# Performance work log

Measured on AMD Instinct MI355X. Metric: run time of the kernel, lower is better.

Reference implementation:

```python
import jax, jax.numpy as jnp
from jax import lax
import numpy as np

NUM_TAGS = 17
B, S = 2048, 512


def setup_inputs() -> dict:
    key = jax.random.key(0)
    k1, k2, k3, k4, k5 = jax.random.split(key, 5)
    inputs = jax.random.normal(k1, (B, S, NUM_TAGS), dtype=jnp.float32)
    tags = jax.random.randint(k2, (B, S), 0, NUM_TAGS, dtype=jnp.int64)
    mask = jnp.ones((B, S), dtype=jnp.int32)
    # learned CRF parameters (xavier-ish / normal init like the torch module)
    transitions = jax.random.normal(k3, (NUM_TAGS, NUM_TAGS), dtype=jnp.float32) * (2.0 / NUM_TAGS) ** 0.5
    start_transitions = jax.random.normal(k4, (NUM_TAGS,), dtype=jnp.float32)
    end_transitions = jax.random.normal(k5, (NUM_TAGS,), dtype=jnp.float32)
    return {"inputs": inputs, "tags": tags, "mask": mask,
            "transitions": transitions,
            "start_transitions": start_transitions,
            "end_transitions": end_transitions}


def _crf_loss(inputs, tags, mask, transitions, start_transitions, end_transitions):
    b, s, t = inputs.shape
    maskf = mask.astype(inputs.dtype)  # (B,S)

    # ---- log partition (denominator): sequential forward recurrence ----
    alpha0 = inputs[:, 0] + start_transitions[None, :]  # (B,T)

    def step(alpha, xm):
        logit_t, m_t = xm  # (B,T), (B,)
        # inner[b,i,j] = alpha[b,i] + emit[b,j] + trans[i,j]
        inner = alpha[:, :, None] + logit_t[:, None, :] + transitions[None, :, :]
        new_alpha = jax.nn.logsumexp(inner, axis=1)  # (B,T)
        alpha = new_alpha * m_t[:, None] + alpha * (1.0 - m_t)[:, None]
        return alpha, None

    xs = (jnp.swapaxes(inputs, 0, 1)[1:], jnp.swapaxes(maskf, 0, 1)[1:])  # (S-1,B,T),(S-1,B)
    alpha, _ = lax.scan(step, alpha0, xs)
    log_denominator = jax.nn.logsumexp(alpha + end_transitions[None, :], axis=-1)  # (B,)

    # ---- gold path score (numerator), fully vectorized over time ----
    score = start_transitions[tags[:, 0]]  # (B,)
    trans_sc = transitions[tags[:, :-1], tags[:, 1:]]  # (B,S-1)
    emit_sc = jnp.take_along_axis(inputs[:, :-1], tags[:, :-1, None], axis=2)[..., 0]  # (B,S-1)
    score = score + jnp.sum(trans_sc * maskf[:, 1:] + emit_sc * maskf[:, :-1], axis=1)
    last_idx = jnp.sum(mask, axis=1).astype(jnp.int32) - 1  # (B,)
    last_tags = jnp.take_along_axis(tags, last_idx[:, None].astype(tags.dtype), axis=1)[:, 0]
    last_input = jnp.take_along_axis(inputs[:, -1], last_tags[:, None], axis=1)[:, 0]
    score = score + end_transitions[last_tags] + last_input * maskf[:, -1]

    return jnp.sum(score - log_denominator)


def reference(inputs, tags, mask, transitions, start_transitions, end_transitions):
    return _crf_loss(inputs, tags, mask, transitions, start_transitions, end_transitions)
```

## Files before the change

### kernel.cpp

```cpp
#include <hip/hip_runtime.h>

#define B_ 2048
#define S_ 512
#define T_ 17
#define REC 40
#define FWDB 64
#define MAINB 128

typedef float v16f __attribute__((ext_vector_type(16)));
typedef short v8s  __attribute__((ext_vector_type(8)));
typedef float f4u  __attribute__((ext_vector_type(4), aligned(4)));

union frag_u { unsigned u[4]; v8s v; };

static __device__ inline unsigned pkbf(float lo, float hi) {
    unsigned r;
    asm volatile("v_cvt_pk_bf16_f32 %0, %1, %2" : "=v"(r) : "v"(lo), "v"(hi));
    return r;
}

#define LOADK(Q0, Q1, SS, MM, T0_) do {                                      \
    const float* bp_ = ip + (size_t)(T0_) * T_;                              \
    _Pragma("unroll") for (int u_ = 0; u_ < 4; ++u_) {                       \
        Q0[u_] = *(const f4u*)(bp_ + u_ * T_ + 4 * h);                       \
        Q1[u_] = *(const f4u*)(bp_ + u_ * T_ + 8 + 4 * h);                   \
        SS[u_] = bp_[u_ * T_ + 16];                                          \
    }                                                                        \
    MM = *(const int4*)(mp + (T0_));                                         \
} while (0)

#define PACKB(S0,S1,S2,S3,S4,S5,S6,S7, BOUT) do {                            \
    unsigned P0_ = pkbf(S0, S1), P1_ = pkbf(S2, S3);                         \
    unsigned R0_ = pkbf(S4, S5), R1_ = pkbf(S6, S7);                         \
    auto s0_ = __builtin_amdgcn_permlane32_swap(P0_, R0_, false, false);     \
    auto s1_ = __builtin_amdgcn_permlane32_swap(P1_, R1_, false, false);     \
    BOUT.u[0] = s0_[0]; BOUT.u[1] = s1_[0];                                  \
    BOUT.u[2] = s0_[1]; BOUT.u[3] = s1_[1];                                  \
} while (0)

#define W16SWAP() do {                                                       \
    auto rw_ = __builtin_amdgcn_permlane32_swap(__float_as_uint(W8),         \
                                                __float_as_uint(W8),         \
                                                false, false);               \
    w16 = __uint_as_float(rw_[0]);                                           \
} while (0)

#define FSTEP(Q0u, Q1u, Su, Mu) do {                                         \
    frag_u Bf_;                                                              \
    PACKB(W0,W1,W2,W3,W4,W5,W6,W7, Bf_);                                     \
    v16f acc_ = __builtin_amdgcn_mfma_f32_32x32x16_bf16(A1.v, Bf_.v, zacc,0,0,0); \
    float d0_=__expf((Q0u).x), d1_=__expf((Q0u).y);                          \
    float d2_=__expf((Q0u).z), d3_=__expf((Q0u).w);                          \
    float d4_=__expf((Q1u).x), d5_=__expf((Q1u).y);                          \
    float d6_=__expf((Q1u).z), d7_=__expf((Q1u).w);                          \
    float d8_=__expf(Su);                                                    \
    bool bm_ = (Mu) != 0;                                                    \
    float n0_ = fmaf(E16[0], w16, acc_[0]) * d0_;                            \
    float n1_ = fmaf(E16[1], w16, acc_[1]) * d1_;                            \
    float n2_ = fmaf(E16[2], w16, acc_[2]) * d2_;                            \
    float n3_ = fmaf(E16[3], w16, acc_[3]) * d3_;                            \
    float n4_ = fmaf(E16[4], w16, acc_[4]) * d4_;                            \
    float n5_ = fmaf(E16[5], w16, acc_[5]) * d5_;                            \
    float n6_ = fmaf(E16[6], w16, acc_[6]) * d6_;                            \
    float n7_ = fmaf(E16[7], w16, acc_[7]) * d7_;                            \
    float n8_ = fmaf(E16[8], w16, acc_[8]) * d8_;                            \
    W0=bm_?n0_:W0; W1=bm_?n1_:W1; W2=bm_?n2_:W2; W3=bm_?n3_:W3;              \
    W4=bm_?n4_:W4; W5=bm_?n5_:W5; W6=bm_?n6_:W6; W7=bm_?n7_:W7;              \
    W8=bm_?n8_:W8;                                                           \
    W16SWAP();                                                               \
} while (0)

#define BSTEP(Q0u, Q1u, Su, Mu) do {                                         \
    float d0_=__expf((Q0u).x), d1_=__expf((Q0u).y);                          \
    float d2_=__expf((Q0u).z), d3_=__expf((Q0u).w);                          \
    float d4_=__expf((Q1u).x), d5_=__expf((Q1u).y);                          \
    float d6_=__expf((Q1u).z), d7_=__expf((Q1u).w);                          \
    float d8_=__expf(Su);                                                    \
    float U16_ = w16 * d8_;                                                  \
    frag_u Bf_;                                                              \
    PACKB(W0*d0_, W1*d1_, W2*d2_, W3*d3_,                                    \
          W4*d4_, W5*d5_, W6*d6_, W7*d7_, Bf_);                              \
    v16f acc_ = __builtin_amdgcn_mfma_f32_32x32x16_bf16(A1.v, Bf_.v, zacc,0,0,0); \
    bool bm_ = (Mu) != 0;                                                    \
    float n0_ = fmaf(E16[0], U16_, acc_[0]);                                 \
    float n1_ = fmaf(E16[1], U16_, acc_[1]);                                 \
    float n2_ = fmaf(E16[2], U16_, acc_[2]);                                 \
    float n3_ = fmaf(E16[3], U16_, acc_[3]);                                 \
    float n4_ = fmaf(E16[4], U16_, acc_[4]);                                 \
    float n5_ = fmaf(E16[5], U16_, acc_[5]);                                 \
    float n6_ = fmaf(E16[6], U16_, acc_[6]);                                 \
    float n7_ = fmaf(E16[7], U16_, acc_[7]);                                 \
    float n8_ = fmaf(E16[8], U16_, acc_[8]);                                 \
    W0=bm_?n0_:W0; W1=bm_?n1_:W1; W2=bm_?n2_:W2; W3=bm_?n3_:W3;              \
    W4=bm_?n4_:W4; W5=bm_?n5_:W5; W6=bm_?n6_:W6; W7=bm_?n7_:W7;              \
    W8=bm_?n8_:W8;                                                           \
    W16SWAP();                                                               \
} while (0)

#define RENORM() do {                                                        \
    float M_ = fmaxf(fmaxf(fmaxf(W0,W1),fmaxf(W2,W3)),                       \
                     fmaxf(fmaxf(W4,W5),fmaxf(fmaxf(W6,W7),W8)));            \
    auto rm_ = __builtin_amdgcn_permlane32_swap(__float_as_uint(M_),         \
                                                __float_as_uint(M_),         \
                                                false, false);               \
    M_ = fmaxf(__uint_as_float(rm_[0]), __uint_as_float(rm_[1]));            \
    float r_ = 1.0f / M_;                                                    \
    Z += __logf(M_);                                                         \
    W0*=r_; W1*=r_; W2*=r_; W3*=r_; W4*=r_;                                  \
    W5*=r_; W6*=r_; W7*=r_; W8*=r_; w16*=r_;                                 \
} while (0)

#define FCHUNK(Q0a, Q1a, Sa, Ma) do {                                        \
    FSTEP(Q0a[0], Q1a[0], Sa[0], (Ma).x);                                    \
    FSTEP(Q0a[1], Q1a[1], Sa[1], (Ma).y);                                    \
    FSTEP(Q0a[2], Q1a[2], Sa[2], (Ma).z);                                    \
    FSTEP(Q0a[3], Q1a[3], Sa[3], (Ma).w);                                    \
    RENORM();                                                                \
} while (0)

#define BCHUNK(Q0a, Q1a, Sa, Ma) do {                                        \
    BSTEP(Q0a[3], Q1a[3], Sa[3], (Ma).w);                                    \
    BSTEP(Q0a[2], Q1a[2], Sa[2], (Ma).z);                                    \
    BSTEP(Q0a[1], Q1a[1], Sa[1], (Ma).y);                                    \
    BSTEP(Q0a[0], Q1a[0], Sa[0], (Ma).x);                                    \
    RENORM();                                                                \
} while (0)

__global__ __launch_bounds__(64) void crf_fused(
    const float* __restrict__ inputs,
    const int*   __restrict__ tags,
    const int*   __restrict__ mask,
    const float* __restrict__ trans,
    const float* __restrict__ startt,
    const float* __restrict__ endt,
    float* __restrict__ ws)
{
    __shared__ float tl[T_ * T_];
    const int lane = (int)threadIdx.x;
    const int bid = (int)blockIdx.x;
    for (int k = lane; k < T_ * T_; k += 64) tl[k] = trans[k];
    __syncthreads();

    if (bid < MAINB) {
        const bool isF = (bid < FWDB);
        const int h = lane >> 5;
        const int col = lane & 31;
        const int seq = (isF ? bid : bid - FWDB) * 32 + col;

        frag_u A1;
#pragma unroll
        for (int wd = 0; wd < 4; ++wd) {
            const int k0 = 8 * h + 2 * wd, k1 = k0 + 1;
            float e0 = 0.0f, e1 = 0.0f;
            if (col < 17) {
                e0 = isF ? __expf(tl[k0 * T_ + col]) : __expf(tl[col * T_ + k0]);
                e1 = isF ? __expf(tl[k1 * T_ + col]) : __expf(tl[col * T_ + k1]);
            }
            A1.u[wd] = pkbf(e0, e1);
        }
        float E16[9];
#pragma unroll
        for (int k = 0; k < 4; ++k) {
            const int r0 = 4 * h + k, r1 = 8 + 4 * h + k;
            E16[k]     = __expf(isF ? tl[16 * T_ + r0] : tl[r0 * T_ + 16]);
            E16[4 + k] = __expf(isF ? tl[16 * T_ + r1] : tl[r1 * T_ + 16]);
        }
        E16[8] = (h == 0) ? __expf(tl[16 * T_ + 16]) : 0.0f;

        v16f zacc;
#pragma unroll
        for (int r = 0; r < 16; ++r) zacc[r] = 0.0f;

        const float* ip = inputs + (size_t)seq * (S_ * T_);
        const int*   mp = mask + (size_t)seq * S_;

        float W0, W1, W2, W3, W4, W5, W6, W7, W8, w16, Z = 0.0f;

        f4u X0[4], X1[4]; float XS[4]; int4 XM;
        f4u Y0[4], Y1[4]; float YS[4]; int4 YM;

        if (isF) {
            LOADK(X0, X1, XS, XM, 0);
            LOADK(Y0, Y1, YS, YM, 4);
            {
                f4u s0 = *(const f4u*)(startt + 4 * h);
                f4u s1 = *(const f4u*)(startt + 8 + 4 * h);
                W0 = __expf(X0[0].x + s0.x); W1 = __expf(X0[0].y + s0.y);
                W2 = __expf(X0[0].z + s0.z); W3 = __expf(X0[0].w + s0.w);
                W4 = __expf(X1[0].x + s1.x); W5 = __expf(X1[0].y + s1.y);
                W6 = __expf(X1[0].z + s1.z); W7 = __expf(X1[0].w + s1.w);
                W8 = h ? 0.0f : __expf(XS[0] + startt[16]);
                W16SWAP();
            }
            FSTEP(X0[1], X1[1], XS[1], XM.y);
            FSTEP(X0[2], X1[2], XS[2], XM.z);
            FSTEP(X0[3], X1[3], XS[3], XM.w);
            RENORM();
            LOADK(X0, X1, XS, XM, 8);
            FCHUNK(Y0, Y1, YS, YM);
            for (int cp = 1; cp < 31; ++cp) {
                LOADK(Y0, Y1, YS, YM, 8 * cp + 4);
                FCHUNK(X0, X1, XS, XM);
                LOADK(X0, X1, XS, XM, 8 * cp + 8);
                FCHUNK(Y0, Y1, YS, YM);
            }
            LOADK(Y0, Y1, YS, YM, 252);
            FCHUNK(X0, X1, XS, XM);
            FCHUNK(Y0, Y1, YS, YM);
            float* rec = ws + (size_t)seq * REC;
            rec[4*h+0] = W0; rec[4*h+1] = W1; rec[4*h+2] = W2; rec[4*h+3] = W3;
            rec[8+4*h+0] = W4; rec[8+4*h+1] = W5; rec[8+4*h+2] = W6; rec[8+4*h+3] = W7;
            if (h == 0) { rec[16] = W8; rec[17] = Z; }
        } else {
            LOADK(X0, X1, XS, XM, 508);
            LOADK(Y0, Y1, YS, YM, 504);
            {
                f4u e0 = *(const f4u*)(endt + 4 * h);
                f4u e1 = *(const f4u*)(endt + 8 + 4 * h);
                W0 = __expf(e0.x); W1 = __expf(e0.y);
                W2 = __expf(e0.z); W3 = __expf(e0.w);
                W4 = __expf(e1.x); W5 = __expf(e1.y);
                W6 = __expf(e1.z); W7 = __expf(e1.w);
                W8 = h ? 0.0f : __expf(endt[16]);
                W16SWAP();
            }
            BCHUNK(X0, X1, XS, XM);
            LOADK(X0, X1, XS, XM, 500);
            BCHUNK(Y0, Y1, YS, YM);
            for (int cp = 1; cp < 31; ++cp) {
                LOADK(Y0, Y1, YS, YM, 508 - 8 * cp - 4);
                BCHUNK(X0, X1, XS, XM);
                LOADK(X0, X1, XS, XM, 508 - 8 * cp - 8);
                BCHUNK(Y0, Y1, YS, YM);
            }
            LOADK(Y0, Y1, YS, YM, 256);
            BCHUNK(X0, X1, XS, XM);
            BCHUNK(Y0, Y1, YS, YM);
            float* rec = ws + (size_t)seq * REC;
            rec[18+4*h+0] = W0; rec[18+4*h+1] = W1;
            rec[18+4*h+2] = W2; rec[18+4*h+3] = W3;
            rec[18+8+4*h+0] = W4; rec[18+8+4*h+1] = W5;
            rec[18+8+4*h+2] = W6; rec[18+8+4*h+3] = W7;
            if (h == 0) { rec[34] = W8; rec[35] = Z; }
        }
    } else {
        const int s = bid - MAINB;
        const int* tp = tags + (size_t)s * S_;
        const int* mp = mask + (size_t)s * S_;
        const float* ib = inputs + (size_t)s * (S_ * T_);
        const int4* tp4 = (const int4*)tp;
        const int4* mp4 = (const int4*)mp;

        int4 t0 = tp4[2 * lane], t1 = tp4[2 * lane + 1];
        int4 m0 = mp4[2 * lane], m1 = mp4[2 * lane + 1];
        int tg[8] = {t0.x, t0.y, t0.z, t0.w, t1.x, t1.y, t1.z, t1.w};
        int mi[8] = {m0.x, m0.y, m0.z, m0.w, m1.x, m1.y, m1.z, m1.w};
        int tprev = (lane > 0) ? tp[8 * lane - 1] : 0;

        float e = 0.0f, tr = 0.0f;
        int ms = 0;
#pragma unroll
        for (int u = 0; u < 8; ++u) {
            int t = 8 * lane + u;
            float mf = (float)mi[u];
            float gate = (t <= S_ - 2) ? mf : 0.0f;
            e = fmaf(gate, ib[(size_t)t * T_ + tg[u]], e);
            int pt = (u == 0) ? tprev : tg[u - 1];
            float tv = tl[pt * T_ + tg[u]];
            tr = fmaf((t >= 1) ? mf : 0.0f, tv, tr);
            ms += mi[u];
        }
        for (int d = 1; d < 64; d <<= 1) {
            e  += __shfl_xor(e, d);
            tr += __shfl_xor(tr, d);
            ms += __shfl_xor(ms, d);
        }
        if (lane == 0) {
            int li = ms - 1; if (li < 0) li = 0;
            int lt = tp[li];
            float ml = (float)mp[S_ - 1];
            float lin = ib[(size_t)(S_ - 1) * T_ + lt];
            float sc = startt[tp[0]] + tr + e + endt[lt] + lin * ml;
            ws[(size_t)s * REC + 36] = sc;
        }
    }
}

__global__ __launch_bounds__(256) void crf_final(const float* __restrict__ ws,
                                                 float* __restrict__ out)
{
    __shared__ float sm[256];
    const int tid = (int)threadIdx.x;
    float a = 0.0f;
    for (int s = tid; s < B_; s += 256) {
        const float* r = ws + (size_t)s * REC;
        float dot = 0.0f;
#pragma unroll
        for (int i = 0; i < T_; ++i) dot = fmaf(r[i], r[18 + i], dot);
        a += r[36] - (r[17] + r[35] + __logf(dot));
    }
    sm[tid] = a;
    __syncthreads();
    for (int k = 128; k >= 1; k >>= 1) {
        if (tid < k) sm[tid] += sm[tid + k];
        __syncthreads();
    }
    if (tid == 0) out[0] = sm[0];
}

extern "C" void kernel_launch(void* const* d_in, const int* in_sizes, int n_in,
                              void* d_out, int out_size, void* d_ws, size_t ws_size,
                              hipStream_t stream)
{
    const float* inputs = (const float*)d_in[0];
    const int*   tags   = (const int*)d_in[1];
    const int*   mask   = (const int*)d_in[2];
    const float* trans  = (const float*)d_in[3];
    const float* startt = (const float*)d_in[4];
    const float* endt   = (const float*)d_in[5];
    float* out = (float*)d_out;
    float* ws  = (float*)d_ws;

    crf_fused<<<MAINB + B_, 64, 0, stream>>>(inputs, tags, mask, trans,
                                             startt, endt, ws);
    crf_final<<<1, 256, 0, stream>>>(ws, out);
}
```

Measured before the change: 67.93 us.

## Interleave forward and backward CRF recurrences in one wavefront

Instead of separate blocks running the forward half and the backward half of each sequence, each wave now runs both chains and alternates their steps. The two independent dependency chains (MFMA, exp, permlane) can then hide each other's latency, and the recurrence needs half as many blocks. The asm volatile qualifier is dropped from the bf16 pack so the compiler can schedule it. The cost is roughly doubled register pressure per wave and fewer waves in flight on the GPU.

```diff
diff --git a/kernel.cpp b/kernel.cpp
--- a/kernel.cpp
+++ b/kernel.cpp
@@ -4,8 +4,7 @@
 #define S_ 512
 #define T_ 17
 #define REC 40
-#define FWDB 64
-#define MAINB 128
+#define MAINB 64
 
 typedef float v16f __attribute__((ext_vector_type(16)));
 typedef short v8s  __attribute__((ext_vector_type(8)));
@@ -15,11 +14,76 @@
 
 static __device__ inline unsigned pkbf(float lo, float hi) {
     unsigned r;
-    asm volatile("v_cvt_pk_bf16_f32 %0, %1, %2" : "=v"(r) : "v"(lo), "v"(hi));
+    asm("v_cvt_pk_bf16_f32 %0, %1, %2" : "=v"(r) : "v"(lo), "v"(hi));
     return r;
 }
 
-#define LOADK(Q0, Q1, SS, MM, T0_) do {                                      \
+#define PACKB(S0,S1,S2,S3,S4,S5,S6,S7, BOUT) do {                            \
+    unsigned P0_ = pkbf(S0, S1), P1_ = pkbf(S2, S3);                         \
+    unsigned R0_ = pkbf(S4, S5), R1_ = pkbf(S6, S7);                         \
+    auto s0_ = __builtin_amdgcn_permlane32_swap(P0_, R0_, false, false);     \
+    auto s1_ = __builtin_amdgcn_permlane32_swap(P1_, R1_, false, false);     \
+    BOUT.u[0] = s0_[0]; BOUT.u[1] = s1_[0];                                  \
+    BOUT.u[2] = s0_[1]; BOUT.u[3] = s1_[1];                                  \
+} while (0)
+
+#define W16SWAPA(W, w16) do {                                                \
+    auto rw_ = __builtin_amdgcn_permlane32_swap(__float_as_uint(W[8]),       \
+                                                __float_as_uint(W[8]),       \
+                                                false, false);               \
+    w16 = __uint_as_float(rw_[0]);                                           \
+} while (0)
+
+#define EXP9(dd_, Q0u, Q1u, Su) do {                                         \
+    dd_[0]=__expf((Q0u).x); dd_[1]=__expf((Q0u).y);                          \
+    dd_[2]=__expf((Q0u).z); dd_[3]=__expf((Q0u).w);                          \
+    dd_[4]=__expf((Q1u).x); dd_[5]=__expf((Q1u).y);                          \
+    dd_[6]=__expf((Q1u).z); dd_[7]=__expf((Q1u).w);                          \
+    dd_[8]=__expf(Su);                                                       \
+} while (0)
+
+#define FSTEPA(W, w16, Z, A1, E16, Q0u, Q1u, Su, Mu) do {                    \
+    frag_u Bf_;                                                              \
+    PACKB(W[0],W[1],W[2],W[3],W[4],W[5],W[6],W[7], Bf_);                     \
+    v16f acc_ = __builtin_amdgcn_mfma_f32_32x32x16_bf16(A1.v, Bf_.v, zacc,0,0,0); \
+    float dd_[9]; EXP9(dd_, Q0u, Q1u, Su);                                   \
+    bool bm_ = (Mu) != 0;                                                    \
+    _Pragma("unroll") for (int k_ = 0; k_ < 9; ++k_) {                       \
+        float n_ = fmaf(E16[k_], w16, acc_[k_]) * dd_[k_];                   \
+        W[k_] = bm_ ? n_ : W[k_];                                            \
+    }                                                                        \
+    W16SWAPA(W, w16);                                                        \
+} while (0)
+
+#define BSTEPA(W, w16, Z, A1, E16, Q0u, Q1u, Su, Mu) do {                    \
+    float dd_[9]; EXP9(dd_, Q0u, Q1u, Su);                                   \
+    float U16_ = w16 * dd_[8];                                               \
+    frag_u Bf_;                                                              \
+    PACKB(W[0]*dd_[0], W[1]*dd_[1], W[2]*dd_[2], W[3]*dd_[3],                \
+          W[4]*dd_[4], W[5]*dd_[5], W[6]*dd_[6], W[7]*dd_[7], Bf_);          \
+    v16f acc_ = __builtin_amdgcn_mfma_f32_32x32x16_bf16(A1.v, Bf_.v, zacc,0,0,0); \
+    bool bm_ = (Mu) != 0;                                                    \
+    _Pragma("unroll") for (int k_ = 0; k_ < 9; ++k_) {                       \
+        float n_ = fmaf(E16[k_], U16_, acc_[k_]);                            \
+        W[k_] = bm_ ? n_ : W[k_];                                            \
+    }                                                                        \
+    W16SWAPA(W, w16);                                                        \
+} while (0)
+
+#define RENORMA(W, w16, Z) do {                                              \
+    float M_ = fmaxf(fmaxf(fmaxf(W[0],W[1]),fmaxf(W[2],W[3])),               \
+                     fmaxf(fmaxf(W[4],W[5]),fmaxf(fmaxf(W[6],W[7]),W[8])));  \
+    auto rm_ = __builtin_amdgcn_permlane32_swap(__float_as_uint(M_),         \
+                                                __float_as_uint(M_),         \
+                                                false, false);               \
+    M_ = fmaxf(__uint_as_float(rm_[0]), __uint_as_float(rm_[1]));            \
+    float r_ = 1.0f / M_;                                                    \
+    Z += __logf(M_);                                                         \
+    _Pragma("unroll") for (int k_ = 0; k_ < 9; ++k_) W[k_] *= r_;            \
+    w16 *= r_;                                                               \
+} while (0)
+
+#define LOADC(Q0, Q1, SS, MM, T0_) do {                                      \
     const float* bp_ = ip + (size_t)(T0_) * T_;                              \
     _Pragma("unroll") for (int u_ = 0; u_ < 4; ++u_) {                       \
         Q0[u_] = *(const f4u*)(bp_ + u_ * T_ + 4 * h);                       \
@@ -29,104 +93,28 @@
     MM = *(const int4*)(mp + (T0_));                                         \
 } while (0)
 
-#define PACKB(S0,S1,S2,S3,S4,S5,S6,S7, BOUT) do {                            \
-    unsigned P0_ = pkbf(S0, S1), P1_ = pkbf(S2, S3);                         \
-    unsigned R0_ = pkbf(S4, S5), R1_ = pkbf(S6, S7);                         \
-    auto s0_ = __builtin_amdgcn_permlane32_swap(P0_, R0_, false, false);     \
-    auto s1_ = __builtin_amdgcn_permlane32_swap(P1_, R1_, false, false);     \
-    BOUT.u[0] = s0_[0]; BOUT.u[1] = s1_[0];                                  \
-    BOUT.u[2] = s0_[1]; BOUT.u[3] = s1_[1];                                  \
-} while (0)
-
-#define W16SWAP() do {                                                       \
-    auto rw_ = __builtin_amdgcn_permlane32_swap(__float_as_uint(W8),         \
-                                                __float_as_uint(W8),         \
-                                                false, false);               \
-    w16 = __uint_as_float(rw_[0]);                                           \
-} while (0)
-
-#define FSTEP(Q0u, Q1u, Su, Mu) do {                                         \
-    frag_u Bf_;                                                              \
-    PACKB(W0,W1,W2,W3,W4,W5,W6,W7, Bf_);                                     \
-    v16f acc_ = __builtin_amdgcn_mfma_f32_32x32x16_bf16(A1.v, Bf_.v, zacc,0,0,0); \
-    float d0_=__expf((Q0u).x), d1_=__expf((Q0u).y);                          \
-    float d2_=__expf((Q0u).z), d3_=__expf((Q0u).w);                          \
-    float d4_=__expf((Q1u).x), d5_=__expf((Q1u).y);                          \
-    float d6_=__expf((Q1u).z), d7_=__expf((Q1u).w);                          \
-    float d8_=__expf(Su);                                                    \
-    bool bm_ = (Mu) != 0;                                                    \
-    float n0_ = fmaf(E16[0], w16, acc_[0]) * d0_;                            \
-    float n1_ = fmaf(E16[1], w16, acc_[1]) * d1_;                            \
-    float n2_ = fmaf(E16[2], w16, acc_[2]) * d2_;                            \
-    float n3_ = fmaf(E16[3], w16, acc_[3]) * d3_;                            \
-    float n4_ = fmaf(E16[4], w16, acc_[4]) * d4_;                            \
-    float n5_ = fmaf(E16[5], w16, acc_[5]) * d5_;                            \
-    float n6_ = fmaf(E16[6], w16, acc_[6]) * d6_;                            \
-    float n7_ = fmaf(E16[7], w16, acc_[7]) * d7_;                            \
-    float n8_ = fmaf(E16[8], w16, acc_[8]) * d8_;                            \
-    W0=bm_?n0_:W0; W1=bm_?n1_:W1; W2=bm_?n2_:W2; W3=bm_?n3_:W3;              \
-    W4=bm_?n4_:W4; W5=bm_?n5_:W5; W6=bm_?n6_:W6; W7=bm_?n7_:W7;              \
-    W8=bm_?n8_:W8;                                                           \
-    W16SWAP();                                                               \
-} while (0)
-
-#define BSTEP(Q0u, Q1u, Su, Mu) do {                                         \
-    float d0_=__expf((Q0u).x), d1_=__expf((Q0u).y);                          \
-    float d2_=__expf((Q0u).z), d3_=__expf((Q0u).w);                          \
-    float d4_=__expf((Q1u).x), d5_=__expf((Q1u).y);                          \
-    float d6_=__expf((Q1u).z), d7_=__expf((Q1u).w);                          \
-    float d8_=__expf(Su);                                                    \
-    float U16_ = w16 * d8_;                                                  \
-    frag_u Bf_;                                                              \
-    PACKB(W0*d0_, W1*d1_, W2*d2_, W3*d3_,                                    \
-          W4*d4_, W5*d5_, W6*d6_, W7*d7_, Bf_);                              \
-    v16f acc_ = __builtin_amdgcn_mfma_f32_32x32x16_bf16(A1.v, Bf_.v, zacc,0,0,0); \
-    bool bm_ = (Mu) != 0;                                                    \
-    float n0_ = fmaf(E16[0], U16_, acc_[0]);                                 \
-    float n1_ = fmaf(E16[1], U16_, acc_[1]);                                 \
-    float n2_ = fmaf(E16[2], U16_, acc_[2]);                                 \
-    float n3_ = fmaf(E16[3], U16_, acc_[3]);                                 \
-    float n4_ = fmaf(E16[4], U16_, acc_[4]);                                 \
-    float n5_ = fmaf(E16[5], U16_, acc_[5]);                                 \
-    float n6_ = fmaf(E16[6], U16_, acc_[6]);                                 \
-    float n7_ = fmaf(E16[7], U16_, acc_[7]);                                 \
-    float n8_ = fmaf(E16[8], U16_, acc_[8]);                                 \
-    W0=bm_?n0_:W0; W1=bm_?n1_:W1; W2=bm_?n2_:W2; W3=bm_?n3_:W3;              \
-    W4=bm_?n4_:W4; W5=bm_?n5_:W5; W6=bm_?n6_:W6; W7=bm_?n7_:W7;              \
-    W8=bm_?n8_:W8;                                                           \
-    W16SWAP();                                                               \
-} while (0)
-
-#define RENORM() do {                                                        \
-    float M_ = fmaxf(fmaxf(fmaxf(W0,W1),fmaxf(W2,W3)),                       \
-                     fmaxf(fmaxf(W4,W5),fmaxf(fmaxf(W6,W7),W8)));            \
-    auto rm_ = __builtin_amdgcn_permlane32_swap(__float_as_uint(M_),         \
-                                                __float_as_uint(M_),         \
-                                                false, false);               \
-    M_ = fmaxf(__uint_as_float(rm_[0]), __uint_as_float(rm_[1]));            \
-    float r_ = 1.0f / M_;                                                    \
-    Z += __logf(M_);                                                         \
-    W0*=r_; W1*=r_; W2*=r_; W3*=r_; W4*=r_;                                  \
-    W5*=r_; W6*=r_; W7*=r_; W8*=r_; w16*=r_;                                 \
-} while (0)
-
-#define FCHUNK(Q0a, Q1a, Sa, Ma) do {                                        \
-    FSTEP(Q0a[0], Q1a[0], Sa[0], (Ma).x);                                    \
-    FSTEP(Q0a[1], Q1a[1], Sa[1], (Ma).y);                                    \
-    FSTEP(Q0a[2], Q1a[2], Sa[2], (Ma).z);                                    \
-    FSTEP(Q0a[3], Q1a[3], Sa[3], (Ma).w);                                    \
-    RENORM();                                                                \
-} while (0)
-
-#define BCHUNK(Q0a, Q1a, Sa, Ma) do {                                        \
-    BSTEP(Q0a[3], Q1a[3], Sa[3], (Ma).w);                                    \
-    BSTEP(Q0a[2], Q1a[2], Sa[2], (Ma).z);                                    \
-    BSTEP(Q0a[1], Q1a[1], Sa[1], (Ma).y);                                    \
-    BSTEP(Q0a[0], Q1a[0], Sa[0], (Ma).x);                                    \
-    RENORM();                                                                \
-} while (0)
-
-__global__ __launch_bounds__(64) void crf_fused(
+#define LOADX(n_) do { LOADC(XP0,XP1,XPS,XPM, 4*(n_));                       \
+                       LOADC(XQ0,XQ1,XQS,XQM, 508-4*(n_)); } while (0)
+#define LOADY(n_) do { LOADC(YP0,YP1,YPS,YPM, 4*(n_));                       \
+                       LOADC(YQ0,YQ1,YQS,YQM, 508-4*(n_)); } while (0)
+
+#define FCH2(P0,P1,PS,PM, Q0,Q1,QS,QM) do {                                  \
+    FSTEPA(WP, wp16, ZP, A1f, E16f, P0[0], P1[0], PS[0], (PM).x);            \
+    BSTEPA(WQ, wq16, ZQ, A1b, E16b, Q0[3], Q1[3], QS[3], (QM).w);            \
+    FSTEPA(WP, wp16, ZP, A1f, E16f, P0[1], P1[1], PS[1], (PM).y);            \
+    BSTEPA(WQ, wq16, ZQ, A1b, E16b, Q0[2], Q1[2], QS[2], (QM).z);            \
+    FSTEPA(WP, wp16, ZP, A1f, E16f, P0[2], P1[2], PS[2], (PM).z);            \
+    BSTEPA(WQ, wq16, ZQ, A1b, E16b, Q0[1], Q1[1], QS[1], (QM).y);            \
+    FSTEPA(WP, wp16, ZP, A1f, E16f, P0[3], P1[3], PS[3], (PM).w);            \
+    BSTEPA(WQ, wq16, ZQ, A1b, E16b, Q0[0], Q1[0], QS[0], (QM).x);            \
+    RENORMA(WP, wp16, ZP);                                                   \
+    RENORMA(WQ, wq16, ZQ);                                                   \
+} while (0)
+
+#define FCHX() FCH2(XP0,XP1,XPS,XPM, XQ0,XQ1,XQS,XQM)
+#define FCHY() FCH2(YP0,YP1,YPS,YPM, YQ0,YQ1,YQS,YQM)
+
+__global__ __launch_bounds__(64, 1) void crf_fused(
     const float* __restrict__ inputs,
     const int*   __restrict__ tags,
     const int*   __restrict__ mask,
@@ -142,30 +130,33 @@
     __syncthreads();
 
     if (bid < MAINB) {
-        const bool isF = (bid < FWDB);
         const int h = lane >> 5;
         const int col = lane & 31;
-        const int seq = (isF ? bid : bid - FWDB) * 32 + col;
-
-        frag_u A1;
+        const int seq = bid * 32 + col;
+
+        frag_u A1f, A1b;
 #pragma unroll
         for (int wd = 0; wd < 4; ++wd) {
             const int k0 = 8 * h + 2 * wd, k1 = k0 + 1;
-            float e0 = 0.0f, e1 = 0.0f;
+            float f0 = 0.0f, f1 = 0.0f, b0 = 0.0f, b1 = 0.0f;
             if (col < 17) {
-                e0 = isF ? __expf(tl[k0 * T_ + col]) : __expf(tl[col * T_ + k0]);
-                e1 = isF ? __expf(tl[k1 * T_ + col]) : __expf(tl[col * T_ + k1]);
+                f0 = __expf(tl[k0 * T_ + col]); f1 = __expf(tl[k1 * T_ + col]);
+                b0 = __expf(tl[col * T_ + k0]); b1 = __expf(tl[col * T_ + k1]);
             }
-            A1.u[wd] = pkbf(e0, e1);
-        }
-        float E16[9];
+            A1f.u[wd] = pkbf(f0, f1);
+            A1b.u[wd] = pkbf(b0, b1);
+        }
+        float E16f[9], E16b[9];
 #pragma unroll
         for (int k = 0; k < 4; ++k) {
             const int r0 = 4 * h + k, r1 = 8 + 4 * h + k;
-            E16[k]     = __expf(isF ? tl[16 * T_ + r0] : tl[r0 * T_ + 16]);
-            E16[4 + k] = __expf(isF ? tl[16 * T_ + r1] : tl[r1 * T_ + 16]);
-        }
-        E16[8] = (h == 0) ? __expf(tl[16 * T_ + 16]) : 0.0f;
+            E16f[k]     = __expf(tl[16 * T_ + r0]);
+            E16f[4 + k] = __expf(tl[16 * T_ + r1]);
+            E16b[k]     = __expf(tl[r0 * T_ + 16]);
+            E16b[4 + k] = __expf(tl[r1 * T_ + 16]);
+        }
+        E16f[8] = (h == 0) ? __expf(tl[16 * T_ + 16]) : 0.0f;
+        E16b[8] = E16f[8];
 
         v16f zacc;
 #pragma unroll
@@ -174,74 +165,68 @@
         const float* ip = inputs + (size_t)seq * (S_ * T_);
         const int*   mp = mask + (size_t)seq * S_;
 
-        float W0, W1, W2, W3, W4, W5, W6, W7, W8, w16, Z = 0.0f;
-
-        f4u X0[4], X1[4]; float XS[4]; int4 XM;
-        f4u Y0[4], Y1[4]; float YS[4]; int4 YM;
-
-        if (isF) {
-            LOADK(X0, X1, XS, XM, 0);
-            LOADK(Y0, Y1, YS, YM, 4);
-            {
-                f4u s0 = *(const f4u*)(startt + 4 * h);
-                f4u s1 = *(const f4u*)(startt + 8 + 4 * h);
-                W0 = __expf(X0[0].x + s0.x); W1 = __expf(X0[0].y + s0.y);
-                W2 = __expf(X0[0].z + s0.z); W3 = __expf(X0[0].w + s0.w);
-                W4 = __expf(X1[0].x + s1.x); W5 = __expf(X1[0].y + s1.y);
-                W6 = __expf(X1[0].z + s1.z); W7 = __expf(X1[0].w + s1.w);
-                W8 = h ? 0.0f : __expf(XS[0] + startt[16]);
-                W16SWAP();
-            }
-            FSTEP(X0[1], X1[1], XS[1], XM.y);
-            FSTEP(X0[2], X1[2], XS[2], XM.z);
-            FSTEP(X0[3], X1[3], XS[3], XM.w);
-            RENORM();
-            LOADK(X0, X1, XS, XM, 8);
-            FCHUNK(Y0, Y1, YS, YM);
-            for (int cp = 1; cp < 31; ++cp) {
-                LOADK(Y0, Y1, YS, YM, 8 * cp + 4);
-                FCHUNK(X0, X1, XS, XM);
-                LOADK(X0, X1, XS, XM, 8 * cp + 8);
-                FCHUNK(Y0, Y1, YS, YM);
-            }
-            LOADK(Y0, Y1, YS, YM, 252);
-            FCHUNK(X0, X1, XS, XM);
-            FCHUNK(Y0, Y1, YS, YM);
-            float* rec = ws + (size_t)seq * REC;
-            rec[4*h+0] = W0; rec[4*h+1] = W1; rec[4*h+2] = W2; rec[4*h+3] = W3;
-            rec[8+4*h+0] = W4; rec[8+4*h+1] = W5; rec[8+4*h+2] = W6; rec[8+4*h+3] = W7;
-            if (h == 0) { rec[16] = W8; rec[17] = Z; }
-        } else {
-            LOADK(X0, X1, XS, XM, 508);
-            LOADK(Y0, Y1, YS, YM, 504);
-            {
-                f4u e0 = *(const f4u*)(endt + 4 * h);
-                f4u e1 = *(const f4u*)(endt + 8 + 4 * h);
-                W0 = __expf(e0.x); W1 = __expf(e0.y);
-                W2 = __expf(e0.z); W3 = __expf(e0.w);
-                W4 = __expf(e1.x); W5 = __expf(e1.y);
-                W6 = __expf(e1.z); W7 = __expf(e1.w);
-                W8 = h ? 0.0f : __expf(endt[16]);
-                W16SWAP();
-            }
-            BCHUNK(X0, X1, XS, XM);
-            LOADK(X0, X1, XS, XM, 500);
-            BCHUNK(Y0, Y1, YS, YM);
-            for (int cp = 1; cp < 31; ++cp) {
-                LOADK(Y0, Y1, YS, YM, 508 - 8 * cp - 4);
-                BCHUNK(X0, X1, XS, XM);
-                LOADK(X0, X1, XS, XM, 508 - 8 * cp - 8);
-                BCHUNK(Y0, Y1, YS, YM);
-            }
-            LOADK(Y0, Y1, YS, YM, 256);
-            BCHUNK(X0, X1, XS, XM);
-            BCHUNK(Y0, Y1, YS, YM);
-            float* rec = ws + (size_t)seq * REC;
-            rec[18+4*h+0] = W0; rec[18+4*h+1] = W1;
-            rec[18+4*h+2] = W2; rec[18+4*h+3] = W3;
-            rec[18+8+4*h+0] = W4; rec[18+8+4*h+1] = W5;
-            rec[18+8+4*h+2] = W6; rec[18+8+4*h+3] = W7;
-            if (h == 0) { rec[34] = W8; rec[35] = Z; }
+        float WP[9], wp16, ZP = 0.0f;
+        float WQ[9], wq16, ZQ = 0.0f;
+
+        f4u XP0[4], XP1[4]; float XPS[4]; int4 XPM;
+        f4u YP0[4], YP1[4]; float YPS[4]; int4 YPM;
+        f4u XQ0[4], XQ1[4]; float XQS[4]; int4 XQM;
+        f4u YQ0[4], YQ1[4]; float YQS[4]; int4 YQM;
+
+        LOADX(0); LOADY(1);
+        {
+            f4u s0 = *(const f4u*)(startt + 4 * h);
+            f4u s1 = *(const f4u*)(startt + 8 + 4 * h);
+            WP[0] = __expf(XP0[0].x + s0.x); WP[1] = __expf(XP0[0].y + s0.y);
+            WP[2] = __expf(XP0[0].z + s0.z); WP[3] = __expf(XP0[0].w + s0.w);
+            WP[4] = __expf(XP1[0].x + s1.x); WP[5] = __expf(XP1[0].y + s1.y);
+            WP[6] = __expf(XP1[0].z + s1.z); WP[7] = __expf(XP1[0].w + s1.w);
+            WP[8] = h ? 0.0f : __expf(XPS[0] + startt[16]);
+            W16SWAPA(WP, wp16);
+        }
+        {
+            f4u e0 = *(const f4u*)(endt + 4 * h);
+            f4u e1 = *(const f4u*)(endt + 8 + 4 * h);
+            WQ[0] = __expf(e0.x); WQ[1] = __expf(e0.y);
+            WQ[2] = __expf(e0.z); WQ[3] = __expf(e0.w);
+            WQ[4] = __expf(e1.x); WQ[5] = __expf(e1.y);
+            WQ[6] = __expf(e1.z); WQ[7] = __expf(e1.w);
+            WQ[8] = h ? 0.0f : __expf(endt[16]);
+            W16SWAPA(WQ, wq16);
+        }
+        FSTEPA(WP, wp16, ZP, A1f, E16f, XP0[1], XP1[1], XPS[1], XPM.y);
+        BSTEPA(WQ, wq16, ZQ, A1b, E16b, XQ0[3], XQ1[3], XQS[3], XQM.w);
+        FSTEPA(WP, wp16, ZP, A1f, E16f, XP0[2], XP1[2], XPS[2], XPM.z);
+        BSTEPA(WQ, wq16, ZQ, A1b, E16b, XQ0[2], XQ1[2], XQS[2], XQM.z);
+        FSTEPA(WP, wp16, ZP, A1f, E16f, XP0[3], XP1[3], XPS[3], XPM.w);
+        BSTEPA(WQ, wq16, ZQ, A1b, E16b, XQ0[1], XQ1[1], XQS[1], XQM.y);
+        BSTEPA(WQ, wq16, ZQ, A1b, E16b, XQ0[0], XQ1[0], XQS[0], XQM.x);
+        RENORMA(WP, wp16, ZP);
+        RENORMA(WQ, wq16, ZQ);
+
+        LOADX(2);
+        FCHY();
+        for (int cp = 1; cp < 31; ++cp) {
+            LOADY(2 * cp + 1);
+            FCHX();
+            LOADX(2 * cp + 2);
+            FCHY();
+        }
+        LOADY(63);
+        FCHX();
+        FCHY();
+
+        float* rec = ws + (size_t)seq * REC;
+#pragma unroll
+        for (int k = 0; k < 4; ++k) {
+            rec[4 * h + k]      = WP[k];
+            rec[8 + 4 * h + k]  = WP[4 + k];
+            rec[18 + 4 * h + k] = WQ[k];
+            rec[26 + 4 * h + k] = WQ[4 + k];
+        }
+        if (h == 0) {
+            rec[16] = WP[8]; rec[17] = ZP;
+            rec[34] = WQ[8]; rec[35] = ZQ;
         }
     } else {
         const int s = bid - MAINB;
```

Measured after the change: 134.0 us. +97.2%, slower.
